# Optimization experiments

Measured on AMD Instinct MI355X. Metric: run time of the kernel, lower is better.

The kernel has to match this reference:

```python
import jax, jax.numpy as jnp
import numpy as np


def setup_inputs() -> dict:
    key = jax.random.key(0)
    kq, kk, kv = jax.random.split(key, 3)
    B, L, H, D = 2, 4096, 8, 64
    queries = jax.random.normal(kq, (B, L, H, D), dtype=jnp.float32)
    keys = jax.random.normal(kk, (B, L, H, D), dtype=jnp.float32)
    values = jax.random.normal(kv, (B, L, H, D), dtype=jnp.float32)
    return {"queries": queries, "keys": keys, "values": values}


def reference(queries, keys, values):
    # queries/keys/values: [B, L, H, D]
    d_model = queries.shape[-1]
    scale = 1.0 / jnp.sqrt(jnp.asarray(d_model, dtype=queries.dtype))
    # scores: [B, H, Lq, Lk]
    scores = jnp.einsum('blhd,bshd->bhls', queries, keys)
    # dropout is identity in eval mode / for deterministic reference
    A = jax.nn.softmax(scale * scores, axis=-1)
    # output: [B, Lq, H, D]
    V = jnp.einsum('bhls,bshd->blhd', A, values)
    return V
```

## Files before the change

### kernel.cpp

```cpp
#include <hip/hip_runtime.h>

#define Bn 2
#define Ln 4096
#define Hn 8
#define Dn 64
#define NMEGA 32
#define BH_STRIDE 262144

typedef float    f32x4 __attribute__((ext_vector_type(4)));
typedef _Float16 f16x4 __attribute__((ext_vector_type(4)));
typedef _Float16 f16x8 __attribute__((ext_vector_type(8)));

static __device__ __forceinline__ void gld16(const void* g, void* l){
    __builtin_amdgcn_global_load_lds(
        (const __attribute__((address_space(1))) unsigned int*)g,
        (__attribute__((address_space(3))) unsigned int*)l, 16, 0, 0);
}

__global__ __launch_bounds__(256)
void kvprep(const float* __restrict__ Kg, const float* __restrict__ Vg,
            _Float16* __restrict__ kp, _Float16* __restrict__ vp){
    __shared__ float tile[64*65];
    const int t = blockIdx.x, bh = blockIdx.y, b = bh>>3, h = bh&7;
    const int tid = threadIdx.x;
#pragma unroll
    for(int i=0;i<2;++i){
        int u = tid + i*256;
        int row = u>>3, blk = (u&7) ^ (row&7);
        const float* src = Kg + (((size_t)b*Ln + t*64 + row)*Hn + h)*Dn + blk*8;
        float4 a = *(const float4*)src;
        float4 c = *(const float4*)(src + 4);
        f16x8 o;
        o[0]=(_Float16)a.x; o[1]=(_Float16)a.y; o[2]=(_Float16)a.z; o[3]=(_Float16)a.w;
        o[4]=(_Float16)c.x; o[5]=(_Float16)c.y; o[6]=(_Float16)c.z; o[7]=(_Float16)c.w;
        *(f16x8*)(kp + (size_t)bh*BH_STRIDE + t*4096 + (size_t)u*8) = o;
    }
#pragma unroll
    for(int i=0;i<4;++i){
        int idx = tid + i*256;
        int k = idx >> 4, d4 = (idx & 15)*4;
        float4 v = *(const float4*)(Vg + (((size_t)b*Ln + t*64 + k)*Hn + h)*Dn + d4);
        tile[k*65 + d4+0]=v.x; tile[k*65+d4+1]=v.y;
        tile[k*65 + d4+2]=v.z; tile[k*65+d4+3]=v.w;
    }
    __syncthreads();
#pragma unroll
    for(int i=0;i<2;++i){
        int u = tid + i*256;
        int d = u>>3, s = u&7;
        int x = s ^ (d&7);
        int lg = x>>1, gh = x&1;
        f16x8 o;
#pragma unroll
        for(int j2=0;j2<8;++j2){
            int g = gh*2 + (j2>>2), j = j2&3;
            int k = g*16 + lg*4 + j;
            o[j2] = (_Float16)tile[k*65 + d];
        }
        *(f16x8*)(vp + (size_t)bh*BH_STRIDE + t*4096 + (size_t)u*8) = o;
    }
}

__global__ __launch_bounds__(256,2)
void attn_fwd(const float* __restrict__ Qg, float* __restrict__ Og,
              const _Float16* __restrict__ kp, const _Float16* __restrict__ vp){
    __shared__ __align__(16) _Float16 sK[2][8192];
    __shared__ __align__(16) _Float16 sV[2][8192];

    const int tid  = threadIdx.x;
    const int lane = tid & 63, wv = tid >> 6;
    const int qh = wv & 1, kh2 = wv >> 1;
    const int ln15 = lane & 15, lg = lane >> 4, ln7 = ln15 & 7;
    const int bh = blockIdx.x, b = bh>>3, h = bh&7;
    const int q0 = blockIdx.y*128 + qh*64;

    const float c = 0.125f * 1.4426950408889634f;

    f16x8 qf[4][2];
#pragma unroll
    for(int qt=0;qt<4;++qt){
        const float* qrow = Qg + (((size_t)b*Ln + q0 + qt*16 + ln15)*Hn + h)*Dn;
#pragma unroll
        for(int ch=0;ch<2;++ch){
            const float* p4 = qrow + ch*32 + lg*8;
            float4 x = *(const float4*)p4;
            float4 y = *(const float4*)(p4+4);
            f16x8 f;
            f[0]=(_Float16)(x.x*c); f[1]=(_Float16)(x.y*c);
            f[2]=(_Float16)(x.z*c); f[3]=(_Float16)(x.w*c);
            f[4]=(_Float16)(y.x*c); f[5]=(_Float16)(y.y*c);
            f[6]=(_Float16)(y.z*c); f[7]=(_Float16)(y.w*c);
            qf[qt][ch]=f;
        }
    }

    f32x4 o[4][4];
    f32x4 lac[4];
#pragma unroll
    for(int qt=0;qt<4;++qt){
        lac[qt] = (f32x4){0.f,0.f,0.f,0.f};
#pragma unroll
        for(int dt=0;dt<4;++dt) o[qt][dt] = (f32x4){0.f,0.f,0.f,0.f};
    }

    const _Float16* kg = kp + (size_t)bh*BH_STRIDE;
    const _Float16* vg = vp + (size_t)bh*BH_STRIDE;

    const int half = kh2*8192;
    const int kb0 = half + ln15*128 + (((0+lg) ^ ln7) << 4);
    const int kb1 = half + ln15*128 + (((4+lg) ^ ln7) << 4);
    int vbofs[2];
#pragma unroll
    for(int gh=0; gh<2; ++gh)
        vbofs[gh] = half + ln15*128 + (((lg*2+gh) ^ ln7) << 4);

#pragma unroll
    for(int i=0;i<4;++i){
        int u = i*256 + tid;
        gld16(kg + (size_t)u*8, &sK[0][(size_t)u*8]);
        gld16(vg + (size_t)u*8, &sV[0][(size_t)u*8]);
    }

    for(int T=0; T<NMEGA; ++T){
        __syncthreads();
        const int cur = T & 1;
        if(T+1 < NMEGA){
            const int nxt = cur ^ 1;
            const _Float16* kgn = kg + (size_t)(T+1)*8192;
            const _Float16* vgn = vg + (size_t)(T+1)*8192;
#pragma unroll
            for(int i=0;i<4;++i){
                int u = i*256 + tid;
                gld16(kgn + (size_t)u*8, &sK[nxt][(size_t)u*8]);
                gld16(vgn + (size_t)u*8, &sV[nxt][(size_t)u*8]);
            }
        }

        f16x8 W[4][2];
#pragma unroll
        for(int dt=0;dt<4;++dt)
#pragma unroll
            for(int gh=0;gh<2;++gh)
                W[dt][gh] = *(const f16x8*)((const char*)&sV[cur][0] + dt*2048 + vbofs[gh]);

#pragma unroll
        for(int g=0; g<4; ++g){
            f16x8 kf0 = *(const f16x8*)((const char*)&sK[cur][0] + g*2048 + kb0);
            f16x8 kf1 = *(const f16x8*)((const char*)&sK[cur][0] + g*2048 + kb1);
#pragma unroll
            for(int qt=0;qt<4;++qt){
                f32x4 s = (f32x4){0.f,0.f,0.f,0.f};
                s = __builtin_amdgcn_mfma_f32_16x16x32_f16(kf0, qf[qt][0], s, 0,0,0);
                s = __builtin_amdgcn_mfma_f32_16x16x32_f16(kf1, qf[qt][1], s, 0,0,0);
                f32x4 p;
                p[0] = __builtin_amdgcn_exp2f(s[0]);
                p[1] = __builtin_amdgcn_exp2f(s[1]);
                p[2] = __builtin_amdgcn_exp2f(s[2]);
                p[3] = __builtin_amdgcn_exp2f(s[3]);
                lac[qt] += p;
                f16x4 pa;
                pa[0]=(_Float16)p[0]; pa[1]=(_Float16)p[1];
                pa[2]=(_Float16)p[2]; pa[3]=(_Float16)p[3];
#pragma unroll
                for(int dt=0;dt<4;++dt){
                    f16x8 Wd = W[dt][g>>1];
                    f16x4 vf = (g & 1)
                        ? __builtin_shufflevector(Wd, Wd, 4,5,6,7)
                        : __builtin_shufflevector(Wd, Wd, 0,1,2,3);
                    o[qt][dt] = __builtin_amdgcn_mfma_f32_16x16x16f16(pa, vf, o[qt][dt], 0,0,0);
                }
            }
        }
    }

    float lred[4];
#pragma unroll
    for(int qt=0;qt<4;++qt){
        float l = (lac[qt][0]+lac[qt][1]) + (lac[qt][2]+lac[qt][3]);
        l += __shfl_xor(l, 16, 64);
        l += __shfl_xor(l, 32, 64);
        lred[qt] = l;
    }

    __syncthreads();
    float* xo = (float*)&sK[0][0];
    float* xl = xo + 2*64*68;
    if(kh2){
#pragma unroll
        for(int qt=0;qt<4;++qt){
#pragma unroll
            for(int dt=0;dt<4;++dt)
#pragma unroll
                for(int r=0;r<4;++r)
                    xo[(qh*64 + qt*16 + lg*4 + r)*68 + dt*16 + ln15] = o[qt][dt][r];
            if(lg==0) xl[qh*64 + qt*16 + ln15] = lred[qt];
        }
    }
    __syncthreads();
    if(!kh2){
#pragma unroll
        for(int qt=0;qt<4;++qt){
            float lt = lred[qt] + xl[qh*64 + qt*16 + ln15];
            float inv = 1.0f/lt;
            float invr[4];
#pragma unroll
            for(int r=0;r<4;++r) invr[r] = __shfl(inv, lg*4 + r, 64);
            float* ob = Og + (((size_t)b*Ln + q0 + qt*16)*Hn + h)*Dn;
#pragma unroll
            for(int dt=0;dt<4;++dt)
#pragma unroll
                for(int r=0;r<4;++r){
                    float val = o[qt][dt][r]
                              + xo[(qh*64 + qt*16 + lg*4 + r)*68 + dt*16 + ln15];
                    ob[(size_t)(lg*4+r)*Hn*Dn + dt*16 + ln15] = val*invr[r];
                }
        }
    }
}

extern "C" void kernel_launch(void* const* d_in, const int* in_sizes, int n_in,
                              void* d_out, int out_size, void* d_ws, size_t ws_size,
                              hipStream_t stream) {
    const float* Q = (const float*)d_in[0];
    const float* K = (const float*)d_in[1];
    const float* V = (const float*)d_in[2];
    float* O = (float*)d_out;

    _Float16* kp = (_Float16*)d_ws;
    _Float16* vp = (_Float16*)((char*)d_ws + (8u<<20));

    kvprep<<<dim3(64, 16), dim3(256), 0, stream>>>(K, V, kp, vp);
    attn_fwd<<<dim3(16, 32), dim3(256), 0, stream>>>(Q, O, kp, vp);
}
```

Before: 169.0 us.

## Switch attention inner loop to 32x32x16 MFMA with permlane32 swap for P

Replaces the 16x16 MFMA tiles for QK^T and PV with 32x32x16 f16 MFMAs. The probability tile is packed with cvt_pkrtz and redistributed between lane halves with permlane32_swap, so it can feed the PV MFMA directly. The K/V preprocessing kernel changes its packed layout to match the new fragment order, which removes the XOR swizzle and lets each lane do one linear 16-byte LDS read. The goal is fewer MFMA issues and LDS reads per key block, at the cost of plain unswizzled LDS access, which may bank-conflict, and a different accumulator register layout.

```diff
diff --git a/kernel.cpp b/kernel.cpp
--- a/kernel.cpp
+++ b/kernel.cpp
@@ -7,14 +7,28 @@
 #define NMEGA 32
 #define BH_STRIDE 262144
 
-typedef float    f32x4 __attribute__((ext_vector_type(4)));
-typedef _Float16 f16x4 __attribute__((ext_vector_type(4)));
-typedef _Float16 f16x8 __attribute__((ext_vector_type(8)));
+typedef float    f32x4  __attribute__((ext_vector_type(4)));
+typedef float    f32x16 __attribute__((ext_vector_type(16)));
+typedef _Float16 f16x2  __attribute__((ext_vector_type(2)));
+typedef _Float16 f16x8  __attribute__((ext_vector_type(8)));
+typedef unsigned int u32;
+typedef u32 u32x2 __attribute__((ext_vector_type(2)));
+typedef u32 u32x4 __attribute__((ext_vector_type(4)));
 
 static __device__ __forceinline__ void gld16(const void* g, void* l){
     __builtin_amdgcn_global_load_lds(
         (const __attribute__((address_space(1))) unsigned int*)g,
         (__attribute__((address_space(3))) unsigned int*)l, 16, 0, 0);
+}
+
+static __device__ __forceinline__ u32 pkf16(float a, float b){
+    auto h = __builtin_amdgcn_cvt_pkrtz(a, b);
+    return __builtin_bit_cast(u32, h);
+}
+
+static __device__ __forceinline__ u32x2 swp(u32 a, u32 b){
+    auto r = __builtin_amdgcn_permlane32_swap(a, b, false, false);
+    return __builtin_bit_cast(u32x2, r);
 }
 
 __global__ __launch_bounds__(256)
@@ -26,38 +40,37 @@
 #pragma unroll
     for(int i=0;i<2;++i){
         int u = tid + i*256;
-        int row = u>>3, blk = (u&7) ^ (row&7);
-        const float* src = Kg + (((size_t)b*Ln + t*64 + row)*Hn + h)*Dn + blk*8;
+        int lane = u & 63, unit = u >> 6;
+        int g = unit >> 2, cc = unit & 3;
+        const float* src = Kg + (((size_t)b*Ln + t*64 + g*32 + (lane&31))*Hn + h)*Dn
+                         + cc*16 + (lane>>5)*8;
         float4 a = *(const float4*)src;
-        float4 c = *(const float4*)(src + 4);
+        float4 c4 = *(const float4*)(src + 4);
         f16x8 o;
-        o[0]=(_Float16)a.x; o[1]=(_Float16)a.y; o[2]=(_Float16)a.z; o[3]=(_Float16)a.w;
-        o[4]=(_Float16)c.x; o[5]=(_Float16)c.y; o[6]=(_Float16)c.z; o[7]=(_Float16)c.w;
-        *(f16x8*)(kp + (size_t)bh*BH_STRIDE + t*4096 + (size_t)u*8) = o;
+        o[0]=(_Float16)a.x;  o[1]=(_Float16)a.y;  o[2]=(_Float16)a.z;  o[3]=(_Float16)a.w;
+        o[4]=(_Float16)c4.x; o[5]=(_Float16)c4.y; o[6]=(_Float16)c4.z; o[7]=(_Float16)c4.w;
+        *(f16x8*)(kp + (size_t)bh*BH_STRIDE + (size_t)t*4096 + (size_t)u*8) = o;
     }
 #pragma unroll
     for(int i=0;i<4;++i){
         int idx = tid + i*256;
         int k = idx >> 4, d4 = (idx & 15)*4;
         float4 v = *(const float4*)(Vg + (((size_t)b*Ln + t*64 + k)*Hn + h)*Dn + d4);
-        tile[k*65 + d4+0]=v.x; tile[k*65+d4+1]=v.y;
-        tile[k*65 + d4+2]=v.z; tile[k*65+d4+3]=v.w;
+        tile[k*65 + d4+0]=v.x; tile[k*65 + d4+1]=v.y;
+        tile[k*65 + d4+2]=v.z; tile[k*65 + d4+3]=v.w;
     }
     __syncthreads();
 #pragma unroll
     for(int i=0;i<2;++i){
         int u = tid + i*256;
-        int d = u>>3, s = u&7;
-        int x = s ^ (d&7);
-        int lg = x>>1, gh = x&1;
+        int lane = u & 63, unit = u >> 6;
+        int g = unit >> 2, kh = (unit >> 1) & 1, dt = unit & 1;
+        int krow = g*32 + kh*16 + (lane>>5)*8;
+        int d = dt*32 + (lane&31);
         f16x8 o;
 #pragma unroll
-        for(int j2=0;j2<8;++j2){
-            int g = gh*2 + (j2>>2), j = j2&3;
-            int k = g*16 + lg*4 + j;
-            o[j2] = (_Float16)tile[k*65 + d];
-        }
-        *(f16x8*)(vp + (size_t)bh*BH_STRIDE + t*4096 + (size_t)u*8) = o;
+        for(int j=0;j<8;++j) o[j] = (_Float16)tile[(krow+j)*65 + d];
+        *(f16x8*)(vp + (size_t)bh*BH_STRIDE + (size_t)t*4096 + (size_t)u*8) = o;
     }
 }
 
@@ -70,19 +83,19 @@
     const int tid  = threadIdx.x;
     const int lane = tid & 63, wv = tid >> 6;
     const int qh = wv & 1, kh2 = wv >> 1;
-    const int ln15 = lane & 15, lg = lane >> 4, ln7 = ln15 & 7;
+    const int l31 = lane & 31, hi = lane >> 5;
     const int bh = blockIdx.x, b = bh>>3, h = bh&7;
     const int q0 = blockIdx.y*128 + qh*64;
 
     const float c = 0.125f * 1.4426950408889634f;
 
-    f16x8 qf[4][2];
-#pragma unroll
-    for(int qt=0;qt<4;++qt){
-        const float* qrow = Qg + (((size_t)b*Ln + q0 + qt*16 + ln15)*Hn + h)*Dn;
-#pragma unroll
-        for(int ch=0;ch<2;++ch){
-            const float* p4 = qrow + ch*32 + lg*8;
+    f16x8 qf[2][4];
+#pragma unroll
+    for(int qt=0;qt<2;++qt){
+        const float* qrow = Qg + (((size_t)b*Ln + q0 + qt*32 + l31)*Hn + h)*Dn;
+#pragma unroll
+        for(int cc=0;cc<4;++cc){
+            const float* p4 = qrow + cc*16 + hi*8;
             float4 x = *(const float4*)p4;
             float4 y = *(const float4*)(p4+4);
             f16x8 f;
@@ -90,29 +103,23 @@
             f[2]=(_Float16)(x.z*c); f[3]=(_Float16)(x.w*c);
             f[4]=(_Float16)(y.x*c); f[5]=(_Float16)(y.y*c);
             f[6]=(_Float16)(y.z*c); f[7]=(_Float16)(y.w*c);
-            qf[qt][ch]=f;
-        }
-    }
-
-    f32x4 o[4][4];
-    f32x4 lac[4];
-#pragma unroll
-    for(int qt=0;qt<4;++qt){
-        lac[qt] = (f32x4){0.f,0.f,0.f,0.f};
-#pragma unroll
-        for(int dt=0;dt<4;++dt) o[qt][dt] = (f32x4){0.f,0.f,0.f,0.f};
-    }
+            qf[qt][cc]=f;
+        }
+    }
+
+    f32x16 o[2][2];
+    float lac[2] = {0.f, 0.f};
+#pragma unroll
+    for(int qt=0;qt<2;++qt)
+#pragma unroll
+        for(int dt=0;dt<2;++dt)
+#pragma unroll
+            for(int r=0;r<16;++r) o[qt][dt][r]=0.f;
 
     const _Float16* kg = kp + (size_t)bh*BH_STRIDE;
     const _Float16* vg = vp + (size_t)bh*BH_STRIDE;
 
-    const int half = kh2*8192;
-    const int kb0 = half + ln15*128 + (((0+lg) ^ ln7) << 4);
-    const int kb1 = half + ln15*128 + (((4+lg) ^ ln7) << 4);
-    int vbofs[2];
-#pragma unroll
-    for(int gh=0; gh<2; ++gh)
-        vbofs[gh] = half + ln15*128 + (((lg*2+gh) ^ ln7) << 4);
+    const int kbyte = kh2*8192 + lane*16;
 
 #pragma unroll
     for(int i=0;i<4;++i){
@@ -136,84 +143,88 @@
             }
         }
 
-        f16x8 W[4][2];
-#pragma unroll
-        for(int dt=0;dt<4;++dt)
-#pragma unroll
-            for(int gh=0;gh<2;++gh)
-                W[dt][gh] = *(const f16x8*)((const char*)&sV[cur][0] + dt*2048 + vbofs[gh]);
-
-#pragma unroll
-        for(int g=0; g<4; ++g){
-            f16x8 kf0 = *(const f16x8*)((const char*)&sK[cur][0] + g*2048 + kb0);
-            f16x8 kf1 = *(const f16x8*)((const char*)&sK[cur][0] + g*2048 + kb1);
-#pragma unroll
-            for(int qt=0;qt<4;++qt){
-                f32x4 s = (f32x4){0.f,0.f,0.f,0.f};
-                s = __builtin_amdgcn_mfma_f32_16x16x32_f16(kf0, qf[qt][0], s, 0,0,0);
-                s = __builtin_amdgcn_mfma_f32_16x16x32_f16(kf1, qf[qt][1], s, 0,0,0);
-                f32x4 p;
-                p[0] = __builtin_amdgcn_exp2f(s[0]);
-                p[1] = __builtin_amdgcn_exp2f(s[1]);
-                p[2] = __builtin_amdgcn_exp2f(s[2]);
-                p[3] = __builtin_amdgcn_exp2f(s[3]);
-                lac[qt] += p;
-                f16x4 pa;
-                pa[0]=(_Float16)p[0]; pa[1]=(_Float16)p[1];
-                pa[2]=(_Float16)p[2]; pa[3]=(_Float16)p[3];
-#pragma unroll
-                for(int dt=0;dt<4;++dt){
-                    f16x8 Wd = W[dt][g>>1];
-                    f16x4 vf = (g & 1)
-                        ? __builtin_shufflevector(Wd, Wd, 4,5,6,7)
-                        : __builtin_shufflevector(Wd, Wd, 0,1,2,3);
-                    o[qt][dt] = __builtin_amdgcn_mfma_f32_16x16x16f16(pa, vf, o[qt][dt], 0,0,0);
+#pragma unroll
+        for(int g=0; g<2; ++g){
+            f16x8 kf[4], vf[2][2];
+#pragma unroll
+            for(int cc=0;cc<4;++cc)
+                kf[cc] = *(const f16x8*)((const char*)&sK[cur][0] + ((g*4+cc)<<10) + kbyte);
+#pragma unroll
+            for(int kh=0;kh<2;++kh)
+#pragma unroll
+                for(int dt=0;dt<2;++dt)
+                    vf[kh][dt] = *(const f16x8*)((const char*)&sV[cur][0]
+                                 + (((g*2+kh)*2+dt)<<10) + kbyte);
+#pragma unroll
+            for(int qt=0;qt<2;++qt){
+                f32x16 s;
+#pragma unroll
+                for(int r=0;r<16;++r) s[r]=0.f;
+                s = __builtin_amdgcn_mfma_f32_32x32x16_f16(kf[0], qf[qt][0], s, 0,0,0);
+                s = __builtin_amdgcn_mfma_f32_32x32x16_f16(kf[1], qf[qt][1], s, 0,0,0);
+                s = __builtin_amdgcn_mfma_f32_32x32x16_f16(kf[2], qf[qt][2], s, 0,0,0);
+                s = __builtin_amdgcn_mfma_f32_32x32x16_f16(kf[3], qf[qt][3], s, 0,0,0);
+#pragma unroll
+                for(int r=0;r<16;++r) s[r] = __builtin_amdgcn_exp2f(s[r]);
+                lac[qt] += ((s[0]+s[1])+(s[2]+s[3])) + ((s[4]+s[5])+(s[6]+s[7]))
+                         + ((s[8]+s[9])+(s[10]+s[11])) + ((s[12]+s[13])+(s[14]+s[15]));
+                u32 A0 = pkf16(s[0],s[1]),   A1 = pkf16(s[2],s[3]);
+                u32 B0 = pkf16(s[4],s[5]),   B1 = pkf16(s[6],s[7]);
+                u32 C0 = pkf16(s[8],s[9]),   C1 = pkf16(s[10],s[11]);
+                u32 D0 = pkf16(s[12],s[13]), D1 = pkf16(s[14],s[15]);
+                u32x2 r0 = swp(A0,B0), r1 = swp(A1,B1);
+                u32x2 r2 = swp(C0,D0), r3 = swp(C1,D1);
+                u32x4 w0 = {r0.x, r1.x, r0.y, r1.y};
+                u32x4 w1 = {r2.x, r3.x, r2.y, r3.y};
+                f16x8 pa0 = __builtin_bit_cast(f16x8, w0);
+                f16x8 pa1 = __builtin_bit_cast(f16x8, w1);
+#pragma unroll
+                for(int dt=0;dt<2;++dt){
+                    o[qt][dt] = __builtin_amdgcn_mfma_f32_32x32x16_f16(pa0, vf[0][dt], o[qt][dt], 0,0,0);
+                    o[qt][dt] = __builtin_amdgcn_mfma_f32_32x32x16_f16(pa1, vf[1][dt], o[qt][dt], 0,0,0);
                 }
             }
         }
     }
 
-    float lred[4];
-#pragma unroll
-    for(int qt=0;qt<4;++qt){
-        float l = (lac[qt][0]+lac[qt][1]) + (lac[qt][2]+lac[qt][3]);
-        l += __shfl_xor(l, 16, 64);
-        l += __shfl_xor(l, 32, 64);
-        lred[qt] = l;
-    }
+    float lred[2];
+#pragma unroll
+    for(int qt=0;qt<2;++qt)
+        lred[qt] = lac[qt] + __shfl_xor(lac[qt], 32, 64);
 
     __syncthreads();
     float* xo = (float*)&sK[0][0];
-    float* xl = xo + 2*64*68;
+    float* xl = xo + 128*68;
     if(kh2){
 #pragma unroll
-        for(int qt=0;qt<4;++qt){
-#pragma unroll
-            for(int dt=0;dt<4;++dt)
-#pragma unroll
-                for(int r=0;r<4;++r)
-                    xo[(qh*64 + qt*16 + lg*4 + r)*68 + dt*16 + ln15] = o[qt][dt][r];
-            if(lg==0) xl[qh*64 + qt*16 + ln15] = lred[qt];
+        for(int qt=0;qt<2;++qt){
+#pragma unroll
+            for(int dt=0;dt<2;++dt)
+#pragma unroll
+                for(int r=0;r<16;++r){
+                    int qr = (r&3) + 8*(r>>2) + 4*hi;
+                    xo[(qh*64 + qt*32 + qr)*68 + dt*32 + l31] = o[qt][dt][r];
+                }
+            if(hi==0) xl[qh*64 + qt*32 + l31] = lred[qt];
         }
     }
     __syncthreads();
     if(!kh2){
 #pragma unroll
-        for(int qt=0;qt<4;++qt){
-            float lt = lred[qt] + xl[qh*64 + qt*16 + ln15];
-            float inv = 1.0f/lt;
-            float invr[4];
-#pragma unroll
-            for(int r=0;r<4;++r) invr[r] = __shfl(inv, lg*4 + r, 64);
-            float* ob = Og + (((size_t)b*Ln + q0 + qt*16)*Hn + h)*Dn;
-#pragma unroll
-            for(int dt=0;dt<4;++dt)
-#pragma unroll
-                for(int r=0;r<4;++r){
+        for(int qt=0;qt<2;++qt){
+            float inv = 1.0f/(lred[qt] + xl[qh*64 + qt*32 + l31]);
+            float* ob = Og + (((size_t)b*Ln + q0 + qt*32)*Hn + h)*Dn;
+#pragma unroll
+            for(int r=0;r<16;++r){
+                int qr = (r&3) + 8*(r>>2) + 4*hi;
+                float invr = __shfl(inv, qr, 64);
+#pragma unroll
+                for(int dt=0;dt<2;++dt){
                     float val = o[qt][dt][r]
-                              + xo[(qh*64 + qt*16 + lg*4 + r)*68 + dt*16 + ln15];
-                    ob[(size_t)(lg*4+r)*Hn*Dn + dt*16 + ln15] = val*invr[r];
+                              + xo[(qh*64 + qt*32 + qr)*68 + dt*32 + l31];
+                    ob[(size_t)qr*Hn*Dn + dt*32 + l31] = val*invr;
                 }
+            }
         }
     }
 }
```

Measured after the change: 168.4 us. No clear change (-0.3%).
